# Optimization experiments

Hardware: AMD Instinct MI355X
Metric: run time of the kernel (lower is better)

Reference implementation:

```python
import jax, jax.numpy as jnp
import numpy as np

NEG_SLOPE = 0.2
LN_EPS = 1e-5


def setup_inputs() -> dict:
    key = jax.random.key(0)
    kx, kw, ks, kd = jax.random.split(key, 4)
    B, T, C, Fin, Fout = 32, 256, 64, 128, 128
    x = jax.random.normal(kx, (B, T, C, Fin), dtype=jnp.float32)
    W = jax.random.normal(kw, (Fin, Fout), dtype=jnp.float32) * (1.0 / np.sqrt(Fin))
    attn_src = jax.random.normal(ks, (Fout,), dtype=jnp.float32) * 0.1
    attn_dst = jax.random.normal(kd, (Fout,), dtype=jnp.float32) * 0.1
    gamma = jnp.ones((Fout,), dtype=jnp.float32)
    beta = jnp.zeros((Fout,), dtype=jnp.float32)
    return {"x": x, "W": W, "attn_src": attn_src, "attn_dst": attn_dst,
            "gamma": gamma, "beta": beta}


def reference(x, W, attn_src, attn_dst, gamma, beta):
    # h: (B,T,C,Fout)
    h = jnp.einsum('btci,io->btco', x, W)
    src = jnp.einsum('btcf,f->btc', h, attn_src)  # score of node as source
    dst = jnp.einsum('btcf,f->btc', h, attn_dst)  # score of node as dest
    # e[b,t,i,j] = src[b,t,i] + dst[b,t,j]
    e = src[..., :, None] + dst[..., None, :]
    e = jnp.where(e >= 0, e, NEG_SLOPE * e)  # leaky_relu
    alpha = jax.nn.softmax(e, axis=-1)       # softmax over neighbors j
    out = jnp.einsum('btij,btjf->btif', alpha, h)
    # LayerNorm over feature dim
    mu = jnp.mean(out, axis=-1, keepdims=True)
    var = jnp.var(out, axis=-1, keepdims=True)
    out = (out - mu) * jax.lax.rsqrt(var + LN_EPS) * gamma + beta
    return jax.nn.relu(out)
```

## Files before the change

### kernel.cpp

```cpp
#include <hip/hip_runtime.h>


typedef __attribute__((ext_vector_type(8))) short short8;
typedef __attribute__((ext_vector_type(4))) float f32x4;

constexpr int   NTILES    = 8192;
constexpr float NEG_SLOPE = 0.2f;
constexpr float LN_EPS    = 1e-5f;

__device__ __forceinline__ unsigned short f2bf(float f) {
    unsigned int u = __builtin_bit_cast(unsigned int, f);
    return (unsigned short)((u + 0x7FFFu + ((u >> 16) & 1u)) >> 16);
}
__device__ __forceinline__ float bf2f(unsigned short h) {
    unsigned int u = (unsigned int)h << 16;
    return __builtin_bit_cast(float, u);
}
__device__ __forceinline__ unsigned swz256(int row, int bytecol) {
    return (unsigned)(row * 256 + bytecol) ^ (unsigned)((row & 7) << 4);
}
__device__ __forceinline__ unsigned swz128(int row, int bytecol) {
    return (unsigned)(row * 128 + bytecol) ^ (unsigned)((row & 7) << 4);
}

__launch_bounds__(256, 2)
__global__ void gat_mfma(const float* __restrict__ x,
                         const float* __restrict__ W,
                         const float* __restrict__ a_src,
                         const float* __restrict__ a_dst,
                         const float* __restrict__ gamma,
                         const float* __restrict__ beta,
                         float* __restrict__ out)
{
    __shared__ unsigned short sWt[128 * 128];
    __shared__ unsigned short sX [64 * 128];
    __shared__ unsigned short sHt[128 * 64];
    __shared__ unsigned short sP [64 * 64];
    __shared__ float s_as[128], s_ad[128], s_g[128], s_b[128];
    __shared__ float s_pS[4][64], s_pD[4][64];
    __shared__ float s_src[64], s_dst[64];

    const int t    = threadIdx.x;
    const int lane = t & 63;
    const int w    = t >> 6;
    const int l15  = lane & 15;
    const int lg   = lane >> 4;

    {
        const float4* W4 = reinterpret_cast<const float4*>(W);
        for (int c = 0; c < 16; ++c) {
            int idx4 = t + 256 * c;
            float4 v = W4[idx4];
            int k  = idx4 >> 5;
            int n0 = (idx4 & 31) << 2;
            *(unsigned short*)((char*)sWt + swz256(n0 + 0, k * 2)) = f2bf(v.x);
            *(unsigned short*)((char*)sWt + swz256(n0 + 1, k * 2)) = f2bf(v.y);
            *(unsigned short*)((char*)sWt + swz256(n0 + 2, k * 2)) = f2bf(v.z);
            *(unsigned short*)((char*)sWt + swz256(n0 + 3, k * 2)) = f2bf(v.w);
        }
        if (t < 128) {
            s_as[t] = a_src[t]; s_ad[t] = a_dst[t];
            s_g[t]  = gamma[t]; s_b[t]  = beta[t];
        }
    }

    for (int tile = blockIdx.x; tile < NTILES; tile += gridDim.x) {
        const float* xb = x   + (size_t)tile * 8192;
        float*       ob = out + (size_t)tile * 8192;

        {
            const float4* x4 = reinterpret_cast<const float4*>(xb);
            #pragma unroll
            for (int c = 0; c < 4; ++c) {
                int idx8 = t + 256 * c;
                float4 v0 = x4[idx8 * 2];
                float4 v1 = x4[idx8 * 2 + 1];
                int m  = idx8 >> 4;
                int k0 = (idx8 & 15) << 3;
                uint4 pk;
                pk.x = (unsigned)f2bf(v0.x) | ((unsigned)f2bf(v0.y) << 16);
                pk.y = (unsigned)f2bf(v0.z) | ((unsigned)f2bf(v0.w) << 16);
                pk.z = (unsigned)f2bf(v1.x) | ((unsigned)f2bf(v1.y) << 16);
                pk.w = (unsigned)f2bf(v1.z) | ((unsigned)f2bf(v1.w) << 16);
                *(uint4*)((char*)sX + swz256(m, k0 * 2)) = pk;
            }
        }
        __syncthreads();

        f32x4 acc[4][2];
        #pragma unroll
        for (int mi = 0; mi < 4; ++mi) {
            acc[mi][0] = f32x4{0.f, 0.f, 0.f, 0.f};
            acc[mi][1] = f32x4{0.f, 0.f, 0.f, 0.f};
        }
        #pragma unroll
        for (int kb = 0; kb < 4; ++kb) {
            const int kbyte = (kb * 32 + lg * 8) * 2;
            short8 bfr0 = *(const short8*)((char*)sWt + swz256(32 * w +  0 + l15, kbyte));
            short8 bfr1 = *(const short8*)((char*)sWt + swz256(32 * w + 16 + l15, kbyte));
            #pragma unroll
            for (int mi = 0; mi < 4; ++mi) {
                short8 afr = *(const short8*)((char*)sX + swz256(mi * 16 + l15, kbyte));
                acc[mi][0] = __builtin_amdgcn_mfma_f32_16x16x32_bf16(afr, bfr0, acc[mi][0], 0, 0, 0);
                acc[mi][1] = __builtin_amdgcn_mfma_f32_16x16x32_bf16(afr, bfr1, acc[mi][1], 0, 0, 0);
            }
        }

        #pragma unroll
        for (int mi = 0; mi < 4; ++mi) {
            const int m0 = mi * 16 + lg * 4;
            #pragma unroll
            for (int nb = 0; nb < 2; ++nb) {
                const int n = 32 * w + nb * 16 + l15;
                uint2 pk;
                pk.x = (unsigned)f2bf(acc[mi][nb][0]) | ((unsigned)f2bf(acc[mi][nb][1]) << 16);
                pk.y = (unsigned)f2bf(acc[mi][nb][2]) | ((unsigned)f2bf(acc[mi][nb][3]) << 16);
                *(uint2*)((char*)sHt + swz128(n, m0 * 2)) = pk;
            }
        }
        __syncthreads();

        {
            const int i = t & 63, p = t >> 6;
            float ps = 0.f, pd = 0.f;
            #pragma unroll 8
            for (int q = 0; q < 32; ++q) {
                const int n = 32 * p + q;
                float hv = bf2f(*(const unsigned short*)((char*)sHt + swz128(n, i * 2)));
                ps = fmaf(hv, s_as[n], ps);
                pd = fmaf(hv, s_ad[n], pd);
            }
            s_pS[p][i] = ps; s_pD[p][i] = pd;
        }
        __syncthreads();
        if (t < 64) {
            s_src[t] = s_pS[0][t] + s_pS[1][t] + s_pS[2][t] + s_pS[3][t];
            s_dst[t] = s_pD[0][t] + s_pD[1][t] + s_pD[2][t] + s_pD[3][t];
        }
        __syncthreads();

        {
            const int i = t >> 2, jg = t & 3;
            const float srci = s_src[i];
            float e[16];
            float mx = -1e30f;
            #pragma unroll
            for (int q = 0; q < 16; ++q) {
                float v = srci + s_dst[jg * 16 + q];
                v = (v >= 0.f) ? v : NEG_SLOPE * v;
                e[q] = v;
                mx = fmaxf(mx, v);
            }
            mx = fmaxf(mx, __shfl_xor(mx, 1, 64));
            mx = fmaxf(mx, __shfl_xor(mx, 2, 64));
            float sm = 0.f;
            #pragma unroll
            for (int q = 0; q < 16; ++q) { e[q] = __expf(e[q] - mx); sm += e[q]; }
            sm += __shfl_xor(sm, 1, 64);
            sm += __shfl_xor(sm, 2, 64);
            const float inv = 1.0f / sm;
            unsigned short a_[16];
            #pragma unroll
            for (int q = 0; q < 16; ++q) a_[q] = f2bf(e[q] * inv);
            uint4 pk0, pk1;
            pk0.x = (unsigned)a_[0]  | ((unsigned)a_[1]  << 16);
            pk0.y = (unsigned)a_[2]  | ((unsigned)a_[3]  << 16);
            pk0.z = (unsigned)a_[4]  | ((unsigned)a_[5]  << 16);
            pk0.w = (unsigned)a_[6]  | ((unsigned)a_[7]  << 16);
            pk1.x = (unsigned)a_[8]  | ((unsigned)a_[9]  << 16);
            pk1.y = (unsigned)a_[10] | ((unsigned)a_[11] << 16);
            pk1.z = (unsigned)a_[12] | ((unsigned)a_[13] << 16);
            pk1.w = (unsigned)a_[14] | ((unsigned)a_[15] << 16);
            *(uint4*)((char*)sP + swz128(i, jg * 32))      = pk0;
            *(uint4*)((char*)sP + swz128(i, jg * 32 + 16)) = pk1;
        }
        __syncthreads();

        f32x4 o[8];
        #pragma unroll
        for (int mi = 0; mi < 8; ++mi) o[mi] = f32x4{0.f, 0.f, 0.f, 0.f};
        #pragma unroll
        for (int kb = 0; kb < 2; ++kb) {
            const int jbyte = (kb * 32 + lg * 8) * 2;
            short8 bfr = *(const short8*)((char*)sP + swz128(w * 16 + l15, jbyte));
            #pragma unroll
            for (int mi = 0; mi < 8; ++mi) {
                short8 afr = *(const short8*)((char*)sHt + swz128(mi * 16 + l15, jbyte));
                o[mi] = __builtin_amdgcn_mfma_f32_16x16x32_bf16(afr, bfr, o[mi], 0, 0, 0);
            }
        }

        float sm1 = 0.f, sm2 = 0.f;
        #pragma unroll
        for (int mi = 0; mi < 8; ++mi)
            #pragma unroll
            for (int r = 0; r < 4; ++r) { float v = o[mi][r]; sm1 += v; sm2 += v * v; }
        sm1 += __shfl_xor(sm1, 16, 64); sm2 += __shfl_xor(sm2, 16, 64);
        sm1 += __shfl_xor(sm1, 32, 64); sm2 += __shfl_xor(sm2, 32, 64);
        const float mu   = sm1 * (1.f / 128.f);
        const float var  = sm2 * (1.f / 128.f) - mu * mu;
        const float rstd = rsqrtf(var + LN_EPS);

        float* orow = ob + (w * 16 + l15) * 128;
        #pragma unroll
        for (int mi = 0; mi < 8; ++mi) {
            const int n0 = mi * 16 + lg * 4;
            float4 gv = *(const float4*)&s_g[n0];
            float4 bv = *(const float4*)&s_b[n0];
            float4 vo;
            vo.x = fmaxf((o[mi][0] - mu) * rstd * gv.x + bv.x, 0.f);
            vo.y = fmaxf((o[mi][1] - mu) * rstd * gv.y + bv.y, 0.f);
            vo.z = fmaxf((o[mi][2] - mu) * rstd * gv.z + bv.z, 0.f);
            vo.w = fmaxf((o[mi][3] - mu) * rstd * gv.w + bv.w, 0.f);
            *(float4*)(orow + n0) = vo;
        }
    }
}

extern "C" void kernel_launch(void* const* d_in, const int* in_sizes, int n_in,
                              void* d_out, int out_size, void* d_ws, size_t ws_size,
                              hipStream_t stream) {
    const float* x   = (const float*)d_in[0];
    const float* W   = (const float*)d_in[1];
    const float* asv = (const float*)d_in[2];
    const float* adv = (const float*)d_in[3];
    const float* gm  = (const float*)d_in[4];
    const float* bt  = (const float*)d_in[5];
    float* out = (float*)d_out;

    hipLaunchKernelGGL(gat_mfma, dim3(512), dim3(256), 0, stream,
                       x, W, asv, adv, gm, bt, out);
}
```

Measured before the change: 119.1 us.

## Keep W fragments in registers, fold attention vectors into W, prefetch next tile

Holds the bf16 W MFMA fragments in registers instead of shared memory, which frees about 32KB of LDS and allows three blocks per CU with a 768-block grid. Computes the src and dst scores directly from fp32 x using the precomputed products W·a_src and W·a_dst, which removes the separate score pass over sHt and two barriers. Prefetches the next tile's x into registers while the current tile is computed, so global loads overlap the MFMA work. This costs more registers, and the scores are now computed from fp32 x rather than from bf16-rounded h, so they differ slightly numerically.

```diff
diff --git a/kernel.cpp b/kernel.cpp
--- a/kernel.cpp
+++ b/kernel.cpp
@@ -5,6 +5,7 @@
 typedef __attribute__((ext_vector_type(4))) float f32x4;
 
 constexpr int   NTILES    = 8192;
+constexpr int   GRID      = 768;
 constexpr float NEG_SLOPE = 0.2f;
 constexpr float LN_EPS    = 1e-5f;
 
@@ -12,10 +13,6 @@
     unsigned int u = __builtin_bit_cast(unsigned int, f);
     return (unsigned short)((u + 0x7FFFu + ((u >> 16) & 1u)) >> 16);
 }
-__device__ __forceinline__ float bf2f(unsigned short h) {
-    unsigned int u = (unsigned int)h << 16;
-    return __builtin_bit_cast(float, u);
-}
 __device__ __forceinline__ unsigned swz256(int row, int bytecol) {
     return (unsigned)(row * 256 + bytecol) ^ (unsigned)((row & 7) << 4);
 }
@@ -23,22 +20,24 @@
     return (unsigned)(row * 128 + bytecol) ^ (unsigned)((row & 7) << 4);
 }
 
-__launch_bounds__(256, 2)
-__global__ void gat_mfma(const float* __restrict__ x,
-                         const float* __restrict__ W,
-                         const float* __restrict__ a_src,
-                         const float* __restrict__ a_dst,
-                         const float* __restrict__ gamma,
-                         const float* __restrict__ beta,
-                         float* __restrict__ out)
+__launch_bounds__(256, 3)
+__global__ void gat_mfma4(const float* __restrict__ x,
+                          const float* __restrict__ W,
+                          const float* __restrict__ a_src,
+                          const float* __restrict__ a_dst,
+                          const float* __restrict__ gamma,
+                          const float* __restrict__ beta,
+                          float* __restrict__ out)
 {
-    __shared__ unsigned short sWt[128 * 128];
-    __shared__ unsigned short sX [64 * 128];
-    __shared__ unsigned short sHt[128 * 64];
-    __shared__ unsigned short sP [64 * 64];
-    __shared__ float s_as[128], s_ad[128], s_g[128], s_b[128];
-    __shared__ float s_pS[4][64], s_pD[4][64];
-    __shared__ float s_src[64], s_dst[64];
+    __shared__ __align__(16) unsigned short sX [64 * 128];
+    __shared__ __align__(16) unsigned short sHt[128 * 64];
+    __shared__ __align__(16) unsigned short sP [64 * 64];
+    __shared__ __align__(16) float s_src[64];
+    __shared__ __align__(16) float s_dst[64];
+    __shared__ __align__(16) float s_ws[128];
+    __shared__ __align__(16) float s_wd[128];
+    __shared__ __align__(16) float s_g[128];
+    __shared__ __align__(16) float s_b[128];
 
     const int t    = threadIdx.x;
     const int lane = t & 63;
@@ -46,66 +45,110 @@
     const int l15  = lane & 15;
     const int lg   = lane >> 4;
 
+    if (t < 128) {
+        const float4* W4  = reinterpret_cast<const float4*>(W) + t * 32;
+        const float4* as4 = reinterpret_cast<const float4*>(a_src);
+        const float4* ad4 = reinterpret_cast<const float4*>(a_dst);
+        float ws = 0.f, wd = 0.f;
+        for (int n4 = 0; n4 < 32; ++n4) {
+            float4 wr = W4[n4], as = as4[n4], ad = ad4[n4];
+            ws += wr.x*as.x + wr.y*as.y + wr.z*as.z + wr.w*as.w;
+            wd += wr.x*ad.x + wr.y*ad.y + wr.z*ad.z + wr.w*ad.w;
+        }
+        s_ws[t] = ws; s_wd[t] = wd;
+        s_g[t] = gamma[t]; s_b[t] = beta[t];
+    }
+
+    short8 wfrag[2][4];
+    #pragma unroll
+    for (int nb = 0; nb < 2; ++nb) {
+        #pragma unroll
+        for (int kb = 0; kb < 4; ++kb) {
+            const int n = 32 * w + nb * 16 + l15;
+            float v[8];
+            #pragma unroll
+            for (int q = 0; q < 8; ++q)
+                v[q] = W[(kb * 32 + lg * 8 + q) * 128 + n];
+            uint4 p;
+            p.x = (unsigned)f2bf(v[0]) | ((unsigned)f2bf(v[1]) << 16);
+            p.y = (unsigned)f2bf(v[2]) | ((unsigned)f2bf(v[3]) << 16);
+            p.z = (unsigned)f2bf(v[4]) | ((unsigned)f2bf(v[5]) << 16);
+            p.w = (unsigned)f2bf(v[6]) | ((unsigned)f2bf(v[7]) << 16);
+            wfrag[nb][kb] = __builtin_bit_cast(short8, p);
+        }
+    }
+    __syncthreads();
+
+    float wsr[8], wdr[8];
     {
-        const float4* W4 = reinterpret_cast<const float4*>(W);
-        for (int c = 0; c < 16; ++c) {
-            int idx4 = t + 256 * c;
-            float4 v = W4[idx4];
-            int k  = idx4 >> 5;
-            int n0 = (idx4 & 31) << 2;
-            *(unsigned short*)((char*)sWt + swz256(n0 + 0, k * 2)) = f2bf(v.x);
-            *(unsigned short*)((char*)sWt + swz256(n0 + 1, k * 2)) = f2bf(v.y);
-            *(unsigned short*)((char*)sWt + swz256(n0 + 2, k * 2)) = f2bf(v.z);
-            *(unsigned short*)((char*)sWt + swz256(n0 + 3, k * 2)) = f2bf(v.w);
-        }
-        if (t < 128) {
-            s_as[t] = a_src[t]; s_ad[t] = a_dst[t];
-            s_g[t]  = gamma[t]; s_b[t]  = beta[t];
-        }
-    }
-
-    for (int tile = blockIdx.x; tile < NTILES; tile += gridDim.x) {
-        const float* xb = x   + (size_t)tile * 8192;
-        float*       ob = out + (size_t)tile * 8192;
-
-        {
-            const float4* x4 = reinterpret_cast<const float4*>(xb);
+        const int k0 = (t & 15) * 8;
+        #pragma unroll
+        for (int q = 0; q < 8; ++q) { wsr[q] = s_ws[k0 + q]; wdr[q] = s_wd[k0 + q]; }
+    }
+
+    float4 px[8];
+    {
+        const float4* x4 = reinterpret_cast<const float4*>(x + (size_t)blockIdx.x * 8192);
+        #pragma unroll
+        for (int c = 0; c < 4; ++c) {
+            const int idx8 = t + 256 * c;
+            px[2*c]   = x4[idx8 * 2];
+            px[2*c+1] = x4[idx8 * 2 + 1];
+        }
+    }
+
+    for (int tile = blockIdx.x; tile < NTILES; tile += GRID) {
+        float* ob = out + (size_t)tile * 8192;
+
+        #pragma unroll
+        for (int c = 0; c < 4; ++c) {
+            const float4 v0 = px[2*c], v1 = px[2*c+1];
+            float ps = v0.x*wsr[0] + v0.y*wsr[1] + v0.z*wsr[2] + v0.w*wsr[3]
+                     + v1.x*wsr[4] + v1.y*wsr[5] + v1.z*wsr[6] + v1.w*wsr[7];
+            float pd = v0.x*wdr[0] + v0.y*wdr[1] + v0.z*wdr[2] + v0.w*wdr[3]
+                     + v1.x*wdr[4] + v1.y*wdr[5] + v1.z*wdr[6] + v1.w*wdr[7];
+            uint4 pk;
+            pk.x = (unsigned)f2bf(v0.x) | ((unsigned)f2bf(v0.y) << 16);
+            pk.y = (unsigned)f2bf(v0.z) | ((unsigned)f2bf(v0.w) << 16);
+            pk.z = (unsigned)f2bf(v1.x) | ((unsigned)f2bf(v1.y) << 16);
+            pk.w = (unsigned)f2bf(v1.z) | ((unsigned)f2bf(v1.w) << 16);
+            const int m = (t >> 4) + 16 * c;
+            *(uint4*)((char*)sX + swz256(m, (t & 15) * 16)) = pk;
+            #pragma unroll
+            for (int msk = 1; msk < 16; msk <<= 1) {
+                ps += __shfl_xor(ps, msk, 64);
+                pd += __shfl_xor(pd, msk, 64);
+            }
+            if ((t & 15) == 0) { s_src[m] = ps; s_dst[m] = pd; }
+        }
+        __syncthreads();
+
+        if (tile + GRID < NTILES) {
+            const float4* xn = reinterpret_cast<const float4*>(x + (size_t)(tile + GRID) * 8192);
             #pragma unroll
             for (int c = 0; c < 4; ++c) {
-                int idx8 = t + 256 * c;
-                float4 v0 = x4[idx8 * 2];
-                float4 v1 = x4[idx8 * 2 + 1];
-                int m  = idx8 >> 4;
-                int k0 = (idx8 & 15) << 3;
-                uint4 pk;
-                pk.x = (unsigned)f2bf(v0.x) | ((unsigned)f2bf(v0.y) << 16);
-                pk.y = (unsigned)f2bf(v0.z) | ((unsigned)f2bf(v0.w) << 16);
-                pk.z = (unsigned)f2bf(v1.x) | ((unsigned)f2bf(v1.y) << 16);
-                pk.w = (unsigned)f2bf(v1.z) | ((unsigned)f2bf(v1.w) << 16);
-                *(uint4*)((char*)sX + swz256(m, k0 * 2)) = pk;
-            }
-        }
-        __syncthreads();
+                const int idx8 = t + 256 * c;
+                px[2*c]   = xn[idx8 * 2];
+                px[2*c+1] = xn[idx8 * 2 + 1];
+            }
+        }
 
         f32x4 acc[4][2];
         #pragma unroll
         for (int mi = 0; mi < 4; ++mi) {
-            acc[mi][0] = f32x4{0.f, 0.f, 0.f, 0.f};
-            acc[mi][1] = f32x4{0.f, 0.f, 0.f, 0.f};
+            acc[mi][0] = f32x4{0.f,0.f,0.f,0.f};
+            acc[mi][1] = f32x4{0.f,0.f,0.f,0.f};
         }
         #pragma unroll
         for (int kb = 0; kb < 4; ++kb) {
-            const int kbyte = (kb * 32 + lg * 8) * 2;
-            short8 bfr0 = *(const short8*)((char*)sWt + swz256(32 * w +  0 + l15, kbyte));
-            short8 bfr1 = *(const short8*)((char*)sWt + swz256(32 * w + 16 + l15, kbyte));
+            const int kbyte = kb * 64 + lg * 16;
             #pragma unroll
             for (int mi = 0; mi < 4; ++mi) {
                 short8 afr = *(const short8*)((char*)sX + swz256(mi * 16 + l15, kbyte));
-                acc[mi][0] = __builtin_amdgcn_mfma_f32_16x16x32_bf16(afr, bfr0, acc[mi][0], 0, 0, 0);
-                acc[mi][1] = __builtin_amdgcn_mfma_f32_16x16x32_bf16(afr, bfr1, acc[mi][1], 0, 0, 0);
-            }
-        }
-
+                acc[mi][0] = __builtin_amdgcn_mfma_f32_16x16x32_bf16(afr, wfrag[0][kb], acc[mi][0], 0, 0, 0);
+                acc[mi][1] = __builtin_amdgcn_mfma_f32_16x16x32_bf16(afr, wfrag[1][kb], acc[mi][1], 0, 0, 0);
+            }
+        }
         #pragma unroll
         for (int mi = 0; mi < 4; ++mi) {
             const int m0 = mi * 16 + lg * 4;
@@ -117,25 +160,6 @@
                 pk.y = (unsigned)f2bf(acc[mi][nb][2]) | ((unsigned)f2bf(acc[mi][nb][3]) << 16);
                 *(uint2*)((char*)sHt + swz128(n, m0 * 2)) = pk;
             }
-        }
-        __syncthreads();
-
-        {
-            const int i = t & 63, p = t >> 6;
-            float ps = 0.f, pd = 0.f;
-            #pragma unroll 8
-            for (int q = 0; q < 32; ++q) {
-                const int n = 32 * p + q;
-                float hv = bf2f(*(const unsigned short*)((char*)sHt + swz128(n, i * 2)));
-                ps = fmaf(hv, s_as[n], ps);
-                pd = fmaf(hv, s_ad[n], pd);
-            }
-            s_pS[p][i] = ps; s_pD[p][i] = pd;
-        }
-        __syncthreads();
-        if (t < 64) {
-            s_src[t] = s_pS[0][t] + s_pS[1][t] + s_pS[2][t] + s_pS[3][t];
-            s_dst[t] = s_pD[0][t] + s_pD[1][t] + s_pD[2][t] + s_pD[3][t];
         }
         __syncthreads();
 
@@ -178,10 +202,10 @@
 
         f32x4 o[8];
         #pragma unroll
-        for (int mi = 0; mi < 8; ++mi) o[mi] = f32x4{0.f, 0.f, 0.f, 0.f};
+        for (int mi = 0; mi < 8; ++mi) o[mi] = f32x4{0.f,0.f,0.f,0.f};
         #pragma unroll
         for (int kb = 0; kb < 2; ++kb) {
-            const int jbyte = (kb * 32 + lg * 8) * 2;
+            const int jbyte = kb * 64 + lg * 16;
             short8 bfr = *(const short8*)((char*)sP + swz128(w * 16 + l15, jbyte));
             #pragma unroll
             for (int mi = 0; mi < 8; ++mi) {
@@ -192,9 +216,10 @@
 
         float sm1 = 0.f, sm2 = 0.f;
         #pragma unroll
-        for (int mi = 0; mi < 8; ++mi)
-            #pragma unroll
-            for (int r = 0; r < 4; ++r) { float v = o[mi][r]; sm1 += v; sm2 += v * v; }
+        for (int mi = 0; mi < 8; ++mi) {
+            #pragma unroll
+            for (int r = 0; r < 4; ++r) { const float v = o[mi][r]; sm1 += v; sm2 += v * v; }
+        }
         sm1 += __shfl_xor(sm1, 16, 64); sm2 += __shfl_xor(sm2, 16, 64);
         sm1 += __shfl_xor(sm1, 32, 64); sm2 += __shfl_xor(sm2, 32, 64);
         const float mu   = sm1 * (1.f / 128.f);
@@ -205,8 +230,8 @@
         #pragma unroll
         for (int mi = 0; mi < 8; ++mi) {
             const int n0 = mi * 16 + lg * 4;
-            float4 gv = *(const float4*)&s_g[n0];
-            float4 bv = *(const float4*)&s_b[n0];
+            const float4 gv = *(const float4*)&s_g[n0];
+            const float4 bv = *(const float4*)&s_b[n0];
             float4 vo;
             vo.x = fmaxf((o[mi][0] - mu) * rstd * gv.x + bv.x, 0.f);
             vo.y = fmaxf((o[mi][1] - mu) * rstd * gv.y + bv.y, 0.f);
@@ -228,6 +253,6 @@
     const float* bt  = (const float*)d_in[5];
     float* out = (float*)d_out;
 
-    hipLaunchKernelGGL(gat_mfma, dim3(512), dim3(256), 0, stream,
+    hipLaunchKernelGGL(gat_mfma4, dim3(GRID), dim3(256), 0, stream,
                        x, W, asv, adv, gm, bt, out);
 }
```

Result: slower. 195.6 us (+64.3%).
